# Performance work log

Measured on AMD Instinct MI355X. Metric: run time of the kernel, lower is better.

Reference implementation:

```python
import jax, jax.numpy as jnp
import numpy as np
import math

DIM = 512

def setup_inputs() -> dict:
    key = jax.random.key(0)
    k1, k2, k3, k4 = jax.random.split(key, 4)
    B, SD, SE, D = 32, 512, 512, DIM
    padded_seqs = jax.random.normal(k1, (B, SD, D), dtype=jnp.float32)
    encoder_padded_seqs = jax.random.normal(k2, (B, SE, D), dtype=jnp.float32)
    decoder_mask = jnp.ones((B, SD, 1), dtype=jnp.float32)
    # attention linear: Linear(2*D, D) -> weight (D, 2*D), bias (D,)
    bound = 1.0 / math.sqrt(2 * D)
    W = jax.random.uniform(k3, (D, 2 * D), dtype=jnp.float32, minval=-bound, maxval=bound)
    b = jax.random.uniform(k4, (D,), dtype=jnp.float32, minval=-bound, maxval=bound)
    return {"padded_seqs": padded_seqs, "encoder_padded_seqs": encoder_padded_seqs,
            "decoder_mask": decoder_mask, "W": W, "b": b}

def reference(padded_seqs, encoder_padded_seqs, decoder_mask, W, b):
    D = padded_seqs.shape[-1]
    scale = 1.0 / math.sqrt(D)
    # scores: (B, seq_d, seq_e) via matmul instead of broadcast multiply-sum
    scores = jnp.einsum('bqd,bkd->bqk', padded_seqs, encoder_padded_seqs) * scale
    attention_weights = jax.nn.softmax(scores, axis=2)
    attention_context = jnp.einsum('bqk,bkd->bqd', attention_weights, encoder_padded_seqs)
    cat = jnp.concatenate([padded_seqs, attention_context], axis=2)  # (B, seq_d, 2D)
    attention_masked = jnp.tanh(cat @ W.T + b) * decoder_mask
    return (attention_masked, attention_weights)
```

## Files before the change

kernel.cpp:

```cpp
#include <hip/hip_runtime.h>
#include <math.h>

typedef unsigned short u16;
typedef unsigned int   u32;
typedef __attribute__((ext_vector_type(8))) short bf16x8;
typedef __attribute__((ext_vector_type(4))) unsigned short u16x4;
typedef __attribute__((ext_vector_type(4))) float f32x4;

#define BATCH  32
#define SEQ    512
#define DM     512
#define SQE    (SEQ*DM)

__device__ __forceinline__ float bf2f(u16 u) {
  union { u32 i; float f; } v; v.i = ((u32)u) << 16; return v.f;
}
__device__ __forceinline__ u16 f2bf(float x) {
  union { float f; u32 i; } v; v.f = x;
  u32 r = v.i + 0x7fffu + ((v.i >> 16) & 1u);
  return (u16)(r >> 16);
}

template<bool F32>
__device__ __forceinline__ bf16x8 ld8(const void* p, size_t eoff) {
  if (F32) {
    const float* f = (const float*)p + eoff;
    float4 a = *(const float4*)f;
    float4 b = *(const float4*)(f + 4);
    bf16x8 o;
    o[0] = (short)f2bf(a.x); o[1] = (short)f2bf(a.y);
    o[2] = (short)f2bf(a.z); o[3] = (short)f2bf(a.w);
    o[4] = (short)f2bf(b.x); o[5] = (short)f2bf(b.y);
    o[6] = (short)f2bf(b.z); o[7] = (short)f2bf(b.w);
    return o;
  }
  return *(const bf16x8*)((const u16*)p + eoff);
}

template<bool FALO, bool FAHI, bool FB>
__device__ __forceinline__ void gemm_mainloop(
    const void* Alo, const void* Ahi, int ktlo, int kttot,
    const void* B, int lda, int ldb,
    u16* sA, u16* sB, f32x4 acc[4][4])
{
  const int tid  = threadIdx.x;
  const int lane = tid & 63;
  const int wid  = tid >> 6;
  const int wm = (wid >> 1) * 64;
  const int wn = (wid & 1) * 64;
  const int lm = lane & 15;
  const int lq = lane >> 4;

  const int c0 = tid, c1 = tid + 256;
  const int r0 = c0 >> 2, k0 = (c0 & 3) * 8;
  const int r1 = c1 >> 2, k1 = (c1 & 3) * 8;

  for (int kt = 0; kt < kttot; ++kt) {
    bf16x8 a0, a1;
    if (kt < ktlo) {
      const size_t ao = (size_t)kt * 32;
      a0 = ld8<FALO>(Alo, ao + (size_t)r0 * lda + k0);
      a1 = ld8<FALO>(Alo, ao + (size_t)r1 * lda + k1);
    } else {
      const size_t ao = (size_t)(kt - ktlo) * 32;
      a0 = ld8<FAHI>(Ahi, ao + (size_t)r0 * lda + k0);
      a1 = ld8<FAHI>(Ahi, ao + (size_t)r1 * lda + k1);
    }
    const size_t bo = (size_t)kt * 32;
    bf16x8 b0 = ld8<FB>(B, bo + (size_t)r0 * ldb + k0);
    bf16x8 b1 = ld8<FB>(B, bo + (size_t)r1 * ldb + k1);
    *(bf16x8*)(sA + c0 * 8) = a0;
    *(bf16x8*)(sA + c1 * 8) = a1;
    *(bf16x8*)(sB + c0 * 8) = b0;
    *(bf16x8*)(sB + c1 * 8) = b1;
    __syncthreads();

    bf16x8 af[4], bfv[4];
#pragma unroll
    for (int i = 0; i < 4; ++i) {
      af[i]  = *(const bf16x8*)(sA + (wm + i * 16 + lm) * 32 + lq * 8);
      bfv[i] = *(const bf16x8*)(sB + (wn + i * 16 + lm) * 32 + lq * 8);
    }
#pragma unroll
    for (int i = 0; i < 4; ++i)
#pragma unroll
      for (int j = 0; j < 4; ++j)
        acc[i][j] = __builtin_amdgcn_mfma_f32_16x16x32_bf16(af[i], bfv[j], acc[i][j], 0, 0, 0);
    __syncthreads();
  }
}

__global__ __launch_bounds__(256) void k_cvtW(const float* __restrict__ W,
                                              u16* __restrict__ Wbf)
{
  const int i = (blockIdx.x * 256 + threadIdx.x) * 8;
  float4 a = *(const float4*)(W + i);
  float4 b = *(const float4*)(W + i + 4);
  bf16x8 o;
  o[0] = (short)f2bf(a.x); o[1] = (short)f2bf(a.y);
  o[2] = (short)f2bf(a.z); o[3] = (short)f2bf(a.w);
  o[4] = (short)f2bf(b.x); o[5] = (short)f2bf(b.y);
  o[6] = (short)f2bf(b.z); o[7] = (short)f2bf(b.w);
  *(bf16x8*)(Wbf + i) = o;
}

__global__ __launch_bounds__(256) void k_scores(const float* __restrict__ P,
                                                const float* __restrict__ E,
                                                float* __restrict__ Sc)
{
  __shared__ u16 sA[128 * 32];
  __shared__ u16 sB[128 * 32];
  const int mt = blockIdx.x, nt = blockIdx.y, b = blockIdx.z;
  const float* A  = P + (size_t)b * SQE + (size_t)(mt * 128) * DM;
  const float* Bp = E + (size_t)b * SQE + (size_t)(nt * 128) * DM;
  f32x4 acc[4][4] = {};
  gemm_mainloop<true, true, true>(A, A, 16, 16, Bp, DM, DM, sA, sB, acc);

  const int tid = threadIdx.x, lane = tid & 63, wid = tid >> 6;
  const int wm = (wid >> 1) * 64, wn = (wid & 1) * 64;
  const int lm = lane & 15, lq = lane >> 4;
  const float scale = 0.044194173824159216f;
  float* out = Sc + (size_t)b * SQE + (size_t)(mt * 128) * SEQ + nt * 128;
#pragma unroll
  for (int i = 0; i < 4; ++i)
#pragma unroll
    for (int j = 0; j < 4; ++j)
#pragma unroll
      for (int r = 0; r < 4; ++r)
        out[(size_t)(wm + i * 16 + lq * 4 + r) * SEQ + wn + j * 16 + lm] = acc[i][j][r] * scale;
}

__global__ __launch_bounds__(256) void v_softmax(const float* __restrict__ Sc,
                                                 float* __restrict__ Wt)
{
  const int row  = blockIdx.x * 4 + (threadIdx.x >> 6);
  const int lane = threadIdx.x & 63;
  const float* src = Sc + (size_t)row * SEQ + lane * 8;
  float4 va = *(const float4*)(src);
  float4 vb = *(const float4*)(src + 4);
  float v[8] = {va.x, va.y, va.z, va.w, vb.x, vb.y, vb.z, vb.w};
  float m = v[0];
#pragma unroll
  for (int j = 1; j < 8; ++j) m = fmaxf(m, v[j]);
#pragma unroll
  for (int off = 32; off > 0; off >>= 1) m = fmaxf(m, __shfl_xor(m, off, 64));
  float s = 0.f;
#pragma unroll
  for (int j = 0; j < 8; ++j) { v[j] = __expf(v[j] - m); s += v[j]; }
#pragma unroll
  for (int off = 32; off > 0; off >>= 1) s += __shfl_xor(s, off, 64);
  const float inv = 1.0f / s;
  float* dst = Wt + (size_t)row * SEQ + lane * 8;
  float4 o0 = {v[0] * inv, v[1] * inv, v[2] * inv, v[3] * inv};
  float4 o1 = {v[4] * inv, v[5] * inv, v[6] * inv, v[7] * inv};
  *(float4*)(dst)     = o0;
  *(float4*)(dst + 4) = o1;
}

__global__ __launch_bounds__(256) void k_context(const float* __restrict__ Wt,
                                                 const float* __restrict__ E,
                                                 u16* __restrict__ Ctx)
{
  __shared__ u16 sA[128 * 32];
  __shared__ u16 sB[128 * 32];
  const int mt = blockIdx.x, nt = blockIdx.y, b = blockIdx.z;
  const int tid  = threadIdx.x;
  const int lane = tid & 63;
  const int wid  = tid >> 6;
  const int wm = (wid >> 1) * 64, wn = (wid & 1) * 64;
  const int lm = lane & 15, lq = lane >> 4;

  const float* A = Wt + (size_t)b * SQE + (size_t)(mt * 128) * SEQ;
  const int c0 = tid, c1 = tid + 256;
  const int ar0 = c0 >> 2, ak0 = (c0 & 3) * 8;
  const int ar1 = c1 >> 2, ak1 = (c1 & 3) * 8;
  const int kk = tid & 31;
  const int cb = (tid >> 5) * 16;
  const float* Eb = E + (size_t)b * SQE + nt * 128 + cb;

  f32x4 acc[4][4] = {};
  for (int kt = 0; kt < 16; ++kt) {
    bf16x8 a0 = ld8<true>(A, (size_t)kt * 32 + (size_t)ar0 * SEQ + ak0);
    bf16x8 a1 = ld8<true>(A, (size_t)kt * 32 + (size_t)ar1 * SEQ + ak1);
    const float* src = Eb + (size_t)(kt * 32 + kk) * DM;
    float4 x0 = *(const float4*)(src);
    float4 x1 = *(const float4*)(src + 4);
    float4 x2 = *(const float4*)(src + 8);
    float4 x3 = *(const float4*)(src + 12);
    *(bf16x8*)(sA + c0 * 8) = a0;
    *(bf16x8*)(sA + c1 * 8) = a1;
    float xs[16] = {x0.x,x0.y,x0.z,x0.w, x1.x,x1.y,x1.z,x1.w,
                    x2.x,x2.y,x2.z,x2.w, x3.x,x3.y,x3.z,x3.w};
#pragma unroll
    for (int j = 0; j < 16; ++j)
      sB[(cb + j) * 32 + kk] = f2bf(xs[j]);
    __syncthreads();

    bf16x8 af[4], bfv[4];
#pragma unroll
    for (int i = 0; i < 4; ++i) {
      af[i]  = *(const bf16x8*)(sA + (wm + i * 16 + lm) * 32 + lq * 8);
      bfv[i] = *(const bf16x8*)(sB + (wn + i * 16 + lm) * 32 + lq * 8);
    }
#pragma unroll
    for (int i = 0; i < 4; ++i)
#pragma unroll
      for (int j = 0; j < 4; ++j)
        acc[i][j] = __builtin_amdgcn_mfma_f32_16x16x32_bf16(af[i], bfv[j], acc[i][j], 0, 0, 0);
    __syncthreads();
  }

  u16* out = Ctx + (size_t)b * SQE + (size_t)(mt * 128) * DM + nt * 128;
#pragma unroll
  for (int i = 0; i < 4; ++i)
#pragma unroll
    for (int j = 0; j < 4; ++j)
#pragma unroll
      for (int r = 0; r < 4; ++r)
        out[(size_t)(wm + i * 16 + lq * 4 + r) * DM + wn + j * 16 + lm] = f2bf(acc[i][j][r]);
}

__global__ __launch_bounds__(256) void k_final(const float* __restrict__ P,
                                               const u16* __restrict__ Ctx,
                                               const u16* __restrict__ Wbf,
                                               const float* __restrict__ bias,
                                               const float* __restrict__ mask,
                                               float* __restrict__ Out)
{
  __shared__ u16 sA[128 * 32];
  __shared__ u16 sB[128 * 32];
  const int mt = blockIdx.x, nt = blockIdx.y, b = blockIdx.z;
  const float* Alo = P   + (size_t)b * SQE + (size_t)(mt * 128) * DM;
  const u16*   Ahi = Ctx + (size_t)b * SQE + (size_t)(mt * 128) * DM;
  const u16*   Bp  = Wbf + (size_t)(nt * 128) * 1024;
  f32x4 acc[4][4] = {};
  gemm_mainloop<true, false, false>(Alo, Ahi, 16, 32, Bp, DM, 1024, sA, sB, acc);

  const int tid = threadIdx.x, lane = tid & 63, wid = tid >> 6;
  const int wm = (wid >> 1) * 64, wn = (wid & 1) * 64;
  const int lm = lane & 15, lq = lane >> 4;
  float* out = Out + (size_t)b * SQE + (size_t)(mt * 128) * DM + nt * 128;
#pragma unroll
  for (int i = 0; i < 4; ++i)
#pragma unroll
    for (int r = 0; r < 4; ++r) {
      const int row = wm + i * 16 + lq * 4 + r;
      const float mv = mask[b * SEQ + mt * 128 + row];
#pragma unroll
      for (int j = 0; j < 4; ++j) {
        const int col = wn + j * 16 + lm;
        out[(size_t)row * DM + col] = tanhf(acc[i][j][r] + bias[nt * 128 + col]) * mv;
      }
    }
}

extern "C" void kernel_launch(void* const* d_in, const int* in_sizes, int n_in,
                              void* d_out, int out_size, void* d_ws, size_t ws_size,
                              hipStream_t stream)
{
  int i8a = -1, i8b = -1, iM = -1, iW = -1, iB = -1;
  for (int i = 0; i < n_in; ++i) {
    const int s = in_sizes[i];
    if (s == BATCH * SQE)      { if (i8a < 0) i8a = i; else i8b = i; }
    else if (s == BATCH * SEQ) iM = i;
    else if (s == DM * 1024)   iW = i;
    else if (s == DM)          iB = i;
  }
  if (i8a < 0) i8a = 0;
  if (i8b < 0) i8b = 1;
  if (iM < 0) iM = 2;
  if (iW < 0) iW = 3;
  if (iB < 0) iB = 4;
  const float* P  = (const float*)d_in[i8a];
  const float* E  = (const float*)d_in[i8b];
  const float* Mk = (const float*)d_in[iM];
  const float* W  = (const float*)d_in[iW];
  const float* Bi = (const float*)d_in[iB];

  float* out0 = (float*)d_out;
  float* out1 = out0 + (size_t)BATCH * SQE;

  u16* Ctx = (u16*)d_ws;
  u16* Wbf = Ctx + (size_t)BATCH * SQE;

  dim3 blk(256);
  dim3 gg(4, 4, BATCH);
  k_cvtW   <<<dim3(DM * 1024 / (256 * 8)), blk, 0, stream>>>(W, Wbf);
  k_scores <<<gg, blk, 0, stream>>>(P, E, out0);
  v_softmax<<<dim3(BATCH * SEQ / 4), blk, 0, stream>>>(out0, out1);
  k_context<<<gg, blk, 0, stream>>>(out1, E, Ctx);
  k_final  <<<gg, blk, 0, stream>>>(P, Ctx, Wbf, Bi, Mk, out0);
}
```

Measured before the change: 222.5 us.

## Pre-convert inputs to bf16 and use async global-to-LDS loads in GEMMs

Adds prep kernels that convert P, W and E to bf16, plus a transposed copy of E, before the GEMMs run. The GEMM main loop now moves tiles straight into LDS with global_load_lds instead of converting in registers and storing to shared memory. Softmax also writes a bf16 copy of the weights, placed in the Ebf buffer, which the context GEMM reads, and tanh is replaced by an exp-based approximation. The goal is to halve GEMM operand traffic and drop per-tile conversion, at the cost of extra conversion passes and workspace. Reusing the Ebf buffer for the softmax weights is safe only because the scores kernel has already finished with it.

```diff
diff --git a/kernel.cpp b/kernel.cpp
--- a/kernel.cpp
+++ b/kernel.cpp
@@ -4,43 +4,34 @@
 typedef unsigned short u16;
 typedef unsigned int   u32;
 typedef __attribute__((ext_vector_type(8))) short bf16x8;
-typedef __attribute__((ext_vector_type(4))) unsigned short u16x4;
 typedef __attribute__((ext_vector_type(4))) float f32x4;
 
 #define BATCH  32
 #define SEQ    512
 #define DM     512
 #define SQE    (SEQ*DM)
-
-__device__ __forceinline__ float bf2f(u16 u) {
-  union { u32 i; float f; } v; v.i = ((u32)u) << 16; return v.f;
-}
+#define NBE    ((size_t)BATCH*SQE)
+
 __device__ __forceinline__ u16 f2bf(float x) {
   union { float f; u32 i; } v; v.f = x;
   u32 r = v.i + 0x7fffu + ((v.i >> 16) & 1u);
   return (u16)(r >> 16);
 }
-
-template<bool F32>
-__device__ __forceinline__ bf16x8 ld8(const void* p, size_t eoff) {
-  if (F32) {
-    const float* f = (const float*)p + eoff;
-    float4 a = *(const float4*)f;
-    float4 b = *(const float4*)(f + 4);
-    bf16x8 o;
-    o[0] = (short)f2bf(a.x); o[1] = (short)f2bf(a.y);
-    o[2] = (short)f2bf(a.z); o[3] = (short)f2bf(a.w);
-    o[4] = (short)f2bf(b.x); o[5] = (short)f2bf(b.y);
-    o[6] = (short)f2bf(b.z); o[7] = (short)f2bf(b.w);
-    return o;
-  }
-  return *(const bf16x8*)((const u16*)p + eoff);
-}
-
-template<bool FALO, bool FAHI, bool FB>
-__device__ __forceinline__ void gemm_mainloop(
-    const void* Alo, const void* Ahi, int ktlo, int kttot,
-    const void* B, int lda, int ldb,
+__device__ __forceinline__ float fast_tanh(float x) {
+  float xc = fminf(fmaxf(x, -15.f), 15.f);
+  float e  = __expf(2.f * xc);
+  return (e - 1.f) * __builtin_amdgcn_rcpf(e + 1.f);
+}
+
+__device__ __forceinline__ void async16(const void* g, void* l) {
+  __builtin_amdgcn_global_load_lds(
+      (const __attribute__((address_space(1))) void*)g,
+      (__attribute__((address_space(3))) void*)l, 16, 0, 0);
+}
+
+__device__ __forceinline__ void gemm_bf16(
+    const u16* Alo, const u16* Ahi, int ktlo, int kttot, int lda,
+    const u16* B, int ldb,
     u16* sA, u16* sB, f32x4 acc[4][4])
 {
   const int tid  = threadIdx.x;
@@ -51,70 +42,103 @@
   const int lm = lane & 15;
   const int lq = lane >> 4;
 
-  const int c0 = tid, c1 = tid + 256;
-  const int r0 = c0 >> 2, k0 = (c0 & 3) * 8;
-  const int r1 = c1 >> 2, k1 = (c1 & 3) * 8;
+  const int r0 = tid >> 2, k0 = (tid & 3) * 8;
+  u16* lA0 = sA + (size_t)(wid * 64) * 8;
+  u16* lA1 = sA + (size_t)(256 + wid * 64) * 8;
+  u16* lB0 = sB + (size_t)(wid * 64) * 8;
+  u16* lB1 = sB + (size_t)(256 + wid * 64) * 8;
 
   for (int kt = 0; kt < kttot; ++kt) {
-    bf16x8 a0, a1;
-    if (kt < ktlo) {
-      const size_t ao = (size_t)kt * 32;
-      a0 = ld8<FALO>(Alo, ao + (size_t)r0 * lda + k0);
-      a1 = ld8<FALO>(Alo, ao + (size_t)r1 * lda + k1);
-    } else {
-      const size_t ao = (size_t)(kt - ktlo) * 32;
-      a0 = ld8<FAHI>(Ahi, ao + (size_t)r0 * lda + k0);
-      a1 = ld8<FAHI>(Ahi, ao + (size_t)r1 * lda + k1);
+    const u16* Ab = (kt < ktlo) ? (Alo + (size_t)kt * 32)
+                                : (Ahi + (size_t)(kt - ktlo) * 32);
+    const u16* Bb = B + (size_t)kt * 32;
+    async16(Ab + (size_t)r0        * lda + k0, lA0);
+    async16(Ab + (size_t)(r0 + 64) * lda + k0, lA1);
+    async16(Bb + (size_t)r0        * ldb + k0, lB0);
+    async16(Bb + (size_t)(r0 + 64) * ldb + k0, lB1);
+    __syncthreads();
+
+    bf16x8 af[4], bv[4];
+#pragma unroll
+    for (int i = 0; i < 4; ++i) {
+      af[i] = *(const bf16x8*)(sA + (wm + i * 16 + lm) * 32 + lq * 8);
+      bv[i] = *(const bf16x8*)(sB + (wn + i * 16 + lm) * 32 + lq * 8);
     }
-    const size_t bo = (size_t)kt * 32;
-    bf16x8 b0 = ld8<FB>(B, bo + (size_t)r0 * ldb + k0);
-    bf16x8 b1 = ld8<FB>(B, bo + (size_t)r1 * ldb + k1);
-    *(bf16x8*)(sA + c0 * 8) = a0;
-    *(bf16x8*)(sA + c1 * 8) = a1;
-    *(bf16x8*)(sB + c0 * 8) = b0;
-    *(bf16x8*)(sB + c1 * 8) = b1;
-    __syncthreads();
-
-    bf16x8 af[4], bfv[4];
-#pragma unroll
-    for (int i = 0; i < 4; ++i) {
-      af[i]  = *(const bf16x8*)(sA + (wm + i * 16 + lm) * 32 + lq * 8);
-      bfv[i] = *(const bf16x8*)(sB + (wn + i * 16 + lm) * 32 + lq * 8);
-    }
 #pragma unroll
     for (int i = 0; i < 4; ++i)
 #pragma unroll
       for (int j = 0; j < 4; ++j)
-        acc[i][j] = __builtin_amdgcn_mfma_f32_16x16x32_bf16(af[i], bfv[j], acc[i][j], 0, 0, 0);
+        acc[i][j] = __builtin_amdgcn_mfma_f32_16x16x32_bf16(af[i], bv[j], acc[i][j], 0, 0, 0);
     __syncthreads();
   }
 }
 
-__global__ __launch_bounds__(256) void k_cvtW(const float* __restrict__ W,
-                                              u16* __restrict__ Wbf)
-{
-  const int i = (blockIdx.x * 256 + threadIdx.x) * 8;
-  float4 a = *(const float4*)(W + i);
-  float4 b = *(const float4*)(W + i + 4);
-  bf16x8 o;
-  o[0] = (short)f2bf(a.x); o[1] = (short)f2bf(a.y);
-  o[2] = (short)f2bf(a.z); o[3] = (short)f2bf(a.w);
-  o[4] = (short)f2bf(b.x); o[5] = (short)f2bf(b.y);
-  o[6] = (short)f2bf(b.z); o[7] = (short)f2bf(b.w);
-  *(bf16x8*)(Wbf + i) = o;
-}
-
-__global__ __launch_bounds__(256) void k_scores(const float* __restrict__ P,
-                                                const float* __restrict__ E,
+__global__ __launch_bounds__(256) void k_prepPW(const float* __restrict__ P,
+                                                const float* __restrict__ W,
+                                                u16* __restrict__ Pbf,
+                                                u16* __restrict__ Wbf)
+{
+  size_t base = (size_t)blockIdx.x * 2048 + threadIdx.x * 8;
+  const float* s; u16* d;
+  if (blockIdx.x < 4096) { s = P + base; d = Pbf + base; }
+  else { size_t o = base - (size_t)4096 * 2048; s = W + o; d = Wbf + o; }
+  float4 a = *(const float4*)s;
+  float4 b = *(const float4*)(s + 4);
+  bf16x8 v;
+  v[0] = (short)f2bf(a.x); v[1] = (short)f2bf(a.y);
+  v[2] = (short)f2bf(a.z); v[3] = (short)f2bf(a.w);
+  v[4] = (short)f2bf(b.x); v[5] = (short)f2bf(b.y);
+  v[6] = (short)f2bf(b.z); v[7] = (short)f2bf(b.w);
+  *(bf16x8*)d = v;
+}
+
+__global__ __launch_bounds__(256) void k_prepE(const float* __restrict__ E,
+                                               u16* __restrict__ Ebf,
+                                               u16* __restrict__ EbfT)
+{
+  __shared__ u16 sT[64][72];
+  const int tid = threadIdx.x;
+  const int s0 = blockIdx.x * 64, d0 = blockIdx.y * 64, b = blockIdx.z;
+  const int r = tid >> 2, c = (tid & 3) * 16;
+  const float* src = E + (size_t)b * SQE + (size_t)(s0 + r) * DM + d0 + c;
+  float4 x0 = ((const float4*)src)[0];
+  float4 x1 = ((const float4*)src)[1];
+  float4 x2 = ((const float4*)src)[2];
+  float4 x3 = ((const float4*)src)[3];
+  float xs[16] = {x0.x,x0.y,x0.z,x0.w, x1.x,x1.y,x1.z,x1.w,
+                  x2.x,x2.y,x2.z,x2.w, x3.x,x3.y,x3.z,x3.w};
+  u16 v[16];
+#pragma unroll
+  for (int j = 0; j < 16; ++j) v[j] = f2bf(xs[j]);
+  bf16x8 o0, o1;
+#pragma unroll
+  for (int j = 0; j < 8; ++j) { o0[j] = (short)v[j]; o1[j] = (short)v[8 + j]; }
+  u16* dro = Ebf + (size_t)b * SQE + (size_t)(s0 + r) * DM + d0 + c;
+  *(bf16x8*)dro = o0;
+  *(bf16x8*)(dro + 8) = o1;
+#pragma unroll
+  for (int j = 0; j < 16; ++j) sT[c + j][r] = v[j];
+  __syncthreads();
+  const int dr = tid >> 2, sc = (tid & 3) * 16;
+  bf16x8 t0, t1;
+#pragma unroll
+  for (int j = 0; j < 8; ++j) { t0[j] = (short)sT[dr][sc + j]; t1[j] = (short)sT[dr][sc + 8 + j]; }
+  u16* dst = EbfT + (size_t)b * SQE + (size_t)(d0 + dr) * SEQ + s0 + sc;
+  *(bf16x8*)dst = t0;
+  *(bf16x8*)(dst + 8) = t1;
+}
+
+__global__ __launch_bounds__(256) void k_scores(const u16* __restrict__ Pbf,
+                                                const u16* __restrict__ Ebf,
                                                 float* __restrict__ Sc)
 {
   __shared__ u16 sA[128 * 32];
   __shared__ u16 sB[128 * 32];
   const int mt = blockIdx.x, nt = blockIdx.y, b = blockIdx.z;
-  const float* A  = P + (size_t)b * SQE + (size_t)(mt * 128) * DM;
-  const float* Bp = E + (size_t)b * SQE + (size_t)(nt * 128) * DM;
+  const u16* A = Pbf + (size_t)b * SQE + (size_t)(mt * 128) * DM;
+  const u16* B = Ebf + (size_t)b * SQE + (size_t)(nt * 128) * DM;
   f32x4 acc[4][4] = {};
-  gemm_mainloop<true, true, true>(A, A, 16, 16, Bp, DM, DM, sA, sB, acc);
+  gemm_bf16(A, A, 16, 16, DM, B, DM, sA, sB, acc);
 
   const int tid = threadIdx.x, lane = tid & 63, wid = tid >> 6;
   const int wm = (wid >> 1) * 64, wn = (wid & 1) * 64;
@@ -131,13 +155,14 @@
 }
 
 __global__ __launch_bounds__(256) void v_softmax(const float* __restrict__ Sc,
-                                                 float* __restrict__ Wt)
+                                                 float* __restrict__ Wt,
+                                                 u16* __restrict__ Wtbf)
 {
   const int row  = blockIdx.x * 4 + (threadIdx.x >> 6);
   const int lane = threadIdx.x & 63;
   const float* src = Sc + (size_t)row * SEQ + lane * 8;
-  float4 va = *(const float4*)(src);
-  float4 vb = *(const float4*)(src + 4);
+  float4 va = ((const float4*)src)[0];
+  float4 vb = ((const float4*)src)[1];
   float v[8] = {va.x, va.y, va.z, va.w, vb.x, vb.y, vb.z, vb.w};
   float m = v[0];
 #pragma unroll
@@ -155,61 +180,27 @@
   float4 o1 = {v[4] * inv, v[5] * inv, v[6] * inv, v[7] * inv};
   *(float4*)(dst)     = o0;
   *(float4*)(dst + 4) = o1;
-}
-
-__global__ __launch_bounds__(256) void k_context(const float* __restrict__ Wt,
-                                                 const float* __restrict__ E,
+  bf16x8 ob;
+#pragma unroll
+  for (int j = 0; j < 8; ++j) ob[j] = (short)f2bf(v[j] * inv);
+  *(bf16x8*)(Wtbf + (size_t)row * SEQ + lane * 8) = ob;
+}
+
+__global__ __launch_bounds__(256) void k_context(const u16* __restrict__ Wtbf,
+                                                 const u16* __restrict__ EbfT,
                                                  u16* __restrict__ Ctx)
 {
   __shared__ u16 sA[128 * 32];
   __shared__ u16 sB[128 * 32];
   const int mt = blockIdx.x, nt = blockIdx.y, b = blockIdx.z;
-  const int tid  = threadIdx.x;
-  const int lane = tid & 63;
-  const int wid  = tid >> 6;
+  const u16* A = Wtbf + (size_t)b * SQE + (size_t)(mt * 128) * SEQ;
+  const u16* B = EbfT + (size_t)b * SQE + (size_t)(nt * 128) * SEQ;
+  f32x4 acc[4][4] = {};
+  gemm_bf16(A, A, 16, 16, SEQ, B, SEQ, sA, sB, acc);
+
+  const int tid = threadIdx.x, lane = tid & 63, wid = tid >> 6;
   const int wm = (wid >> 1) * 64, wn = (wid & 1) * 64;
   const int lm = lane & 15, lq = lane >> 4;
-
-  const float* A = Wt + (size_t)b * SQE + (size_t)(mt * 128) * SEQ;
-  const int c0 = tid, c1 = tid + 256;
-  const int ar0 = c0 >> 2, ak0 = (c0 & 3) * 8;
-  const int ar1 = c1 >> 2, ak1 = (c1 & 3) * 8;
-  const int kk = tid & 31;
-  const int cb = (tid >> 5) * 16;
-  const float* Eb = E + (size_t)b * SQE + nt * 128 + cb;
-
-  f32x4 acc[4][4] = {};
-  for (int kt = 0; kt < 16; ++kt) {
-    bf16x8 a0 = ld8<true>(A, (size_t)kt * 32 + (size_t)ar0 * SEQ + ak0);
-    bf16x8 a1 = ld8<true>(A, (size_t)kt * 32 + (size_t)ar1 * SEQ + ak1);
-    const float* src = Eb + (size_t)(kt * 32 + kk) * DM;
-    float4 x0 = *(const float4*)(src);
-    float4 x1 = *(const float4*)(src + 4);
-    float4 x2 = *(const float4*)(src + 8);
-    float4 x3 = *(const float4*)(src + 12);
-    *(bf16x8*)(sA + c0 * 8) = a0;
-    *(bf16x8*)(sA + c1 * 8) = a1;
-    float xs[16] = {x0.x,x0.y,x0.z,x0.w, x1.x,x1.y,x1.z,x1.w,
-                    x2.x,x2.y,x2.z,x2.w, x3.x,x3.y,x3.z,x3.w};
-#pragma unroll
-    for (int j = 0; j < 16; ++j)
-      sB[(cb + j) * 32 + kk] = f2bf(xs[j]);
-    __syncthreads();
-
-    bf16x8 af[4], bfv[4];
-#pragma unroll
-    for (int i = 0; i < 4; ++i) {
-      af[i]  = *(const bf16x8*)(sA + (wm + i * 16 + lm) * 32 + lq * 8);
-      bfv[i] = *(const bf16x8*)(sB + (wn + i * 16 + lm) * 32 + lq * 8);
-    }
-#pragma unroll
-    for (int i = 0; i < 4; ++i)
-#pragma unroll
-      for (int j = 0; j < 4; ++j)
-        acc[i][j] = __builtin_amdgcn_mfma_f32_16x16x32_bf16(af[i], bfv[j], acc[i][j], 0, 0, 0);
-    __syncthreads();
-  }
-
   u16* out = Ctx + (size_t)b * SQE + (size_t)(mt * 128) * DM + nt * 128;
 #pragma unroll
   for (int i = 0; i < 4; ++i)
@@ -220,7 +211,7 @@
         out[(size_t)(wm + i * 16 + lq * 4 + r) * DM + wn + j * 16 + lm] = f2bf(acc[i][j][r]);
 }
 
-__global__ __launch_bounds__(256) void k_final(const float* __restrict__ P,
+__global__ __launch_bounds__(256) void k_final(const u16* __restrict__ Pbf,
                                                const u16* __restrict__ Ctx,
                                                const u16* __restrict__ Wbf,
                                                const float* __restrict__ bias,
@@ -230,11 +221,11 @@
   __shared__ u16 sA[128 * 32];
   __shared__ u16 sB[128 * 32];
   const int mt = blockIdx.x, nt = blockIdx.y, b = blockIdx.z;
-  const float* Alo = P   + (size_t)b * SQE + (size_t)(mt * 128) * DM;
-  const u16*   Ahi = Ctx + (size_t)b * SQE + (size_t)(mt * 128) * DM;
-  const u16*   Bp  = Wbf + (size_t)(nt * 128) * 1024;
+  const u16* Alo = Pbf + (size_t)b * SQE + (size_t)(mt * 128) * DM;
+  const u16* Ahi = Ctx + (size_t)b * SQE + (size_t)(mt * 128) * DM;
+  const u16* B   = Wbf + (size_t)(nt * 128) * 1024;
   f32x4 acc[4][4] = {};
-  gemm_mainloop<true, false, false>(Alo, Ahi, 16, 32, Bp, DM, 1024, sA, sB, acc);
+  gemm_bf16(Alo, Ahi, 16, 32, DM, B, 1024, sA, sB, acc);
 
   const int tid = threadIdx.x, lane = tid & 63, wid = tid >> 6;
   const int wm = (wid >> 1) * 64, wn = (wid & 1) * 64;
@@ -249,7 +240,7 @@
 #pragma unroll
       for (int j = 0; j < 4; ++j) {
         const int col = wn + j * 16 + lm;
-        out[(size_t)row * DM + col] = tanhf(acc[i][j][r] + bias[nt * 128 + col]) * mv;
+        out[(size_t)row * DM + col] = fast_tanh(acc[i][j][r] + bias[nt * 128 + col]) * mv;
       }
     }
 }
@@ -278,16 +269,20 @@
   const float* Bi = (const float*)d_in[iB];
 
   float* out0 = (float*)d_out;
-  float* out1 = out0 + (size_t)BATCH * SQE;
-
-  u16* Ctx = (u16*)d_ws;
-  u16* Wbf = Ctx + (size_t)BATCH * SQE;
+  float* out1 = out0 + NBE;
+
+  u16* Pbf  = (u16*)d_ws;
+  u16* Ebf  = Pbf  + NBE;
+  u16* EbfT = Ebf  + NBE;
+  u16* Ctx  = EbfT + NBE;
+  u16* Wbf  = Ctx  + NBE;
 
   dim3 blk(256);
   dim3 gg(4, 4, BATCH);
-  k_cvtW   <<<dim3(DM * 1024 / (256 * 8)), blk, 0, stream>>>(W, Wbf);
-  k_scores <<<gg, blk, 0, stream>>>(P, E, out0);
-  v_softmax<<<dim3(BATCH * SEQ / 4), blk, 0, stream>>>(out0, out1);
-  k_context<<<gg, blk, 0, stream>>>(out1, E, Ctx);
-  k_final  <<<gg, blk, 0, stream>>>(P, Ctx, Wbf, Bi, Mk, out0);
-}
+  k_prepPW <<<dim3(4352), blk, 0, stream>>>(P, W, Pbf, Wbf);
+  k_prepE  <<<dim3(8, 8, BATCH), blk, 0, stream>>>(E, Ebf, EbfT);
+  k_scores <<<gg, blk, 0, stream>>>(Pbf, Ebf, out0);
+  v_softmax<<<dim3(BATCH * SEQ / 4), blk, 0, stream>>>(out0, out1, Ebf );
+  k_context<<<gg, blk, 0, stream>>>(Ebf , EbfT, Ctx);
+  k_final  <<<gg, blk, 0, stream>>>(Pbf, Ctx, Wbf, Bi, Mk, out0);
+}
```

Measured after the change: 208.3 us. 1.07x faster.
